# Kernel tuning notes

Hardware: AMD Instinct MI355X
Metric: run time of the kernel (lower is better)

The kernel has to match this reference:

```python
import jax, jax.numpy as jnp
import numpy as np

B = 1024
FEATURE_NUM = 13 + 26 * 4000  # 104013 (13 dense + 26 sparse fields, one-hot dim 4000 each)
FIELD_NUM = 13 + 26           # 39
K = 8


def setup_inputs() -> dict:
    key = jax.random.key(0)
    k1, k2, k3 = jax.random.split(key, 3)
    inputs = jax.random.uniform(k1, (B, FEATURE_NUM), dtype=jnp.float32)
    w0 = jnp.zeros((1,), dtype=jnp.float32)
    w = jax.random.normal(k2, (FEATURE_NUM, 1), dtype=jnp.float32) * 0.05
    v = jax.random.normal(k3, (FEATURE_NUM, FIELD_NUM, K), dtype=jnp.float32) * 0.05
    return {"inputs": inputs, "w0": w0, "w": w, "v": v}


def reference(inputs, w0, w, v):
    # linear part: [B, 1]
    linear_part = w0 + inputs @ w
    # field_f: [B, field_num, K] via tensordot over feature axis
    field_f = jnp.tensordot(inputs, v, axes=1)
    # sum over upper triangle (i<j) of <field_f_i, field_f_j> using the
    # sum-square FM identity: 0.5 * (||sum_i f_i||^2 - sum_i ||f_i||^2)
    s = field_f.sum(axis=1)                       # [B, K]
    inter = 0.5 * (jnp.sum(s * s, axis=-1)
                   - jnp.sum(field_f * field_f, axis=(1, 2)))  # [B]
    return linear_part + inter[:, None]           # [B, 1]
```

## Files before the change

kernel.cpp:

```cpp
#include <hip/hip_runtime.h>
#include <stdint.h>

#define B_SZ 1024
#define F_SZ 104013
#define NFIELD 39
#define N_RAW 312
#define N_PAD 320
#define KB_STEPS 3251
#define PART_ELEMS ((size_t)B_SZ * N_PAD)

using bf16x8 = __attribute__((ext_vector_type(8))) short;
using f32x4  = __attribute__((ext_vector_type(4))) float;

typedef __attribute__((address_space(3))) void* lds_vp;
typedef const __attribute__((address_space(1))) void* glb_cvp;

__device__ __forceinline__ void ld16(const void* g, void* l) {
  __builtin_amdgcn_global_load_lds((glb_cvp)g, (lds_vp)l, 16, 0, 0);
}

__device__ __forceinline__ unsigned int pack_bf16(float a, float b) {
  unsigned int ua = __float_as_uint(a) + 0x8000u;
  unsigned int ub = __float_as_uint(b) + 0x8000u;
  return (ua >> 16) | (ub & 0xffff0000u);
}

__global__ __launch_bounds__(256) void pack_v(const float* __restrict__ v,
                                              const float* __restrict__ w,
                                              uint4* __restrict__ Bp) {
  const int kb = blockIdx.x;
  const int t  = threadIdx.x;
  __shared__ float vs[32][324];

  for (int idx = t; idx < 32 * 78; idx += 256) {
    int r = idx / 78, c4 = (idx % 78) * 4;
    int k = kb * 32 + r;
    float4 val = make_float4(0.f, 0.f, 0.f, 0.f);
    if (k < F_SZ) val = *(const float4*)(v + (size_t)k * N_RAW + c4);
    *(float4*)&vs[r][c4] = val;
  }
  if (t < 32) {
    int k = kb * 32 + t;
    vs[t][312] = (k < F_SZ) ? w[k] : 0.f;
#pragma unroll
    for (int c = 313; c < 320; ++c) vs[t][c] = 0.f;
  }
  __syncthreads();

#pragma unroll
  for (int i = 0; i < 5; ++i) {
    int p  = t + 256 * i;
    int l  = p & 63;
    int kr = (l >> 4) * 8;
    int col = (p >> 6) * 16 + (l & 15);
    uint4 o;
    o.x = pack_bf16(vs[kr + 0][col], vs[kr + 1][col]);
    o.y = pack_bf16(vs[kr + 2][col], vs[kr + 3][col]);
    o.z = pack_bf16(vs[kr + 4][col], vs[kr + 5][col]);
    o.w = pack_bf16(vs[kr + 6][col], vs[kr + 7][col]);
    Bp[(size_t)kb * 1280 + p] = o;
  }
}

#define LDS_BUF 30720
#define B_OFF   10240

__global__ __launch_bounds__(512, 2) void gemm_split(const float* __restrict__ A,
                                                     const uint4* __restrict__ Bp,
                                                     float* __restrict__ part) {
  const int S  = gridDim.x;
  const int s  = blockIdx.x, mt = blockIdx.y;
  const int t  = threadIdx.x;
  const int w  = t >> 6, l = t & 63;
  const int wr = w >> 2, wc = w & 3;
  const int lm = l & 15, lq = l >> 4;
  const int row0 = mt * 128;
  const int kb0 = (int)((long long)KB_STEPS * s / S);
  const int kb1 = (int)((long long)KB_STEPS * (s + 1) / S);

  __shared__ __align__(16) char smem[2][LDS_BUF];

  const int srow = t >> 2, seg = t & 3;
  const float* ag = A + (size_t)(row0 + srow) * F_SZ + seg * 8;
  const int wswz = srow * 80 + ((seg ^ (srow & 3)) << 4);

  auto loadA = [&](int kb, float4& d0, float4& d1) {
    const float* ap = ag + (size_t)kb * 32;
    if (kb != KB_STEPS - 1) {
      d0 = *(const float4*)(ap);
      d1 = *(const float4*)(ap + 4);
    } else {
      const int kbase = kb * 32 + seg * 8;
      float f[8];
#pragma unroll
      for (int e = 0; e < 8; ++e) f[e] = (kbase + e < F_SZ) ? ap[e] : 0.f;
      d0 = make_float4(f[0], f[1], f[2], f[3]);
      d1 = make_float4(f[4], f[5], f[6], f[7]);
    }
  };

  auto writeA = [&](int buf, const float4& d0, const float4& d1) {
    uint4 pk;
    pk.x = pack_bf16(d0.x, d0.y);
    pk.y = pack_bf16(d0.z, d0.w);
    pk.z = pack_bf16(d1.x, d1.y);
    pk.w = pack_bf16(d1.z, d1.w);
    *(uint4*)(smem[buf] + wswz) = pk;
  };

  auto stageB = [&](int kb, int buf) {
    for (int c = w; c < 20; c += 8)
      ld16(Bp + ((size_t)kb * 20 + c) * 64 + l, smem[buf] + B_OFF + c * 1024);
  };

  f32x4 acc[4][5];
#pragma unroll
  for (int i = 0; i < 4; ++i)
#pragma unroll
    for (int n = 0; n < 5; ++n) acc[i][n] = (f32x4)0.f;

  auto compute = [&](int buf) {
    const char* bs = smem[buf];
    bf16x8 af[4];
#pragma unroll
    for (int i = 0; i < 4; ++i)
      af[i] = __builtin_bit_cast(
          bf16x8, *(const uint4*)(bs + (wr * 64 + i * 16 + lm) * 80 +
                                  ((lq ^ (lm & 3)) << 4)));
#pragma unroll
    for (int n = 0; n < 5; ++n) {
      bf16x8 bf = __builtin_bit_cast(
          bf16x8, *(const uint4*)(bs + B_OFF + (wc * 5 + n) * 1024 + l * 16));
#pragma unroll
      for (int i = 0; i < 4; ++i)
        acc[i][n] = __builtin_amdgcn_mfma_f32_16x16x32_bf16(af[i], bf,
                                                            acc[i][n], 0, 0, 0);
    }
  };

  float4 a0, a1, b0, b1;
  loadA(kb0, a0, a1);
  stageB(kb0, 0);
  writeA(0, a0, a1);
  if (kb0 + 1 < kb1) loadA(kb0 + 1, b0, b1);
  __syncthreads();

  int kb = kb0, cur = 0;
  while (true) {
    if (kb + 1 < kb1) {
      stageB(kb + 1, cur ^ 1);
      writeA(cur ^ 1, b0, b1);
      if (kb + 2 < kb1) loadA(kb + 2, a0, a1);
    }
    compute(cur);
    __syncthreads();
    ++kb; cur ^= 1;
    if (kb >= kb1) break;

    if (kb + 1 < kb1) {
      stageB(kb + 1, cur ^ 1);
      writeA(cur ^ 1, a0, a1);
      if (kb + 2 < kb1) loadA(kb + 2, b0, b1);
    }
    compute(cur);
    __syncthreads();
    ++kb; cur ^= 1;
    if (kb >= kb1) break;
  }

  float* outp = part + (size_t)s * PART_ELEMS;
#pragma unroll
  for (int i = 0; i < 4; ++i) {
    int rb = row0 + wr * 64 + i * 16 + lq * 4;
#pragma unroll
    for (int n = 0; n < 5; ++n) {
      int col = (wc * 5 + n) * 16 + lm;
#pragma unroll
      for (int r = 0; r < 4; ++r)
        outp[(size_t)(rb + r) * N_PAD + col] = acc[i][n][r];
    }
  }
}

__global__ __launch_bounds__(320) void finalize(const float* __restrict__ part,
                                                const float* __restrict__ w0,
                                                float* __restrict__ out, int S) {
  const int b = blockIdx.x;
  const int t = threadIdx.x;
  __shared__ float crow[N_PAD];
  __shared__ float red[5];
  __shared__ float skl[8];

  float acc = 0.f;
  const float* p = part + (size_t)b * N_PAD + t;
#pragma unroll 4
  for (int s = 0; s < S; ++s) acc += p[(size_t)s * PART_ELEMS];
  crow[t] = acc;

  float sq = (t < N_RAW) ? acc * acc : 0.f;
#pragma unroll
  for (int off = 32; off; off >>= 1) sq += __shfl_down(sq, off);
  if ((t & 63) == 0) red[t >> 6] = sq;
  __syncthreads();

  if (t < 8) {
    float sk = 0.f;
#pragma unroll
    for (int f = 0; f < NFIELD; ++f) sk += crow[f * 8 + t];
    skl[t] = sk;
  }
  __syncthreads();
  if (t == 0) {
    float sumsq = red[0] + red[1] + red[2] + red[3] + red[4];
    float ss = 0.f;
#pragma unroll
    for (int k = 0; k < 8; ++k) ss += skl[k] * skl[k];
    out[b] = w0[0] + crow[312] + 0.5f * (ss - sumsq);
  }
}

extern "C" void kernel_launch(void* const* d_in, const int* in_sizes, int n_in,
                              void* d_out, int out_size, void* d_ws, size_t ws_size,
                              hipStream_t stream) {
  const float* inputs = (const float*)d_in[0];
  const float* w0 = (const float*)d_in[1];
  const float* w  = (const float*)d_in[2];
  const float* v  = (const float*)d_in[3];
  float* out = (float*)d_out;

  const size_t PART_BYTES   = PART_ELEMS * sizeof(float);
  const size_t PACKED_BYTES = (size_t)KB_STEPS * 20 * 64 * 16;
  int S = 32;
  while (S > 1 && PACKED_BYTES + (size_t)S * PART_BYTES > ws_size) S >>= 1;

  float* part = (float*)d_ws;
  uint4* Bp   = (uint4*)((char*)d_ws + (size_t)S * PART_BYTES);

  pack_v<<<dim3(KB_STEPS), 256, 0, stream>>>(v, w, Bp);
  gemm_split<<<dim3(S, 8), 512, 0, stream>>>(inputs, Bp, part);
  finalize<<<dim3(B_SZ), 320, 0, stream>>>(part, w0, out, S);
}
```

Before: 737.0 us.

## Triple-buffer LDS and deepen prefetch pipeline with explicit vmcnt waits

The GEMM main loop moves from double-buffered LDS with a full __syncthreads to three LDS stages. A is prefetched into registers three k-blocks ahead and B is staged two ahead. Barriers become explicit s_waitcnt vmcnt(N) plus s_barrier, so outstanding global loads can stay in flight across iterations. The packed B layout is padded from 20 to 24 chunks per k-block so each wave issues a fixed three async loads, which adds zero padding and more LDS per block (raising the risk of lower occupancy) and more packed-buffer traffic.

```diff
diff --git a/kernel.cpp b/kernel.cpp
--- a/kernel.cpp
+++ b/kernel.cpp
@@ -7,6 +7,7 @@
 #define N_RAW 312
 #define N_PAD 320
 #define KB_STEPS 3251
+#define BCH 24
 #define PART_ELEMS ((size_t)B_SZ * N_PAD)
 
 using bf16x8 = __attribute__((ext_vector_type(8))) short;
@@ -58,12 +59,20 @@
     o.y = pack_bf16(vs[kr + 2][col], vs[kr + 3][col]);
     o.z = pack_bf16(vs[kr + 4][col], vs[kr + 5][col]);
     o.w = pack_bf16(vs[kr + 6][col], vs[kr + 7][col]);
-    Bp[(size_t)kb * 1280 + p] = o;
-  }
-}
-
-#define LDS_BUF 30720
-#define B_OFF   10240
+    Bp[(size_t)kb * (BCH * 64) + p] = o;
+  }
+  Bp[(size_t)kb * (BCH * 64) + 1280 + t] = make_uint4(0u, 0u, 0u, 0u);
+}
+
+#define LDS_A   10240
+#define LDS_BSZ 24576
+#define LDS_BUF (LDS_A + LDS_BSZ)
+
+#define SYNC(N) do {                                                     \
+    asm volatile("s_waitcnt vmcnt(" #N ") lgkmcnt(0)" ::: "memory");     \
+    __builtin_amdgcn_s_barrier();                                        \
+    __builtin_amdgcn_sched_barrier(0);                                   \
+  } while (0)
 
 __global__ __launch_bounds__(512, 2) void gemm_split(const float* __restrict__ A,
                                                      const uint4* __restrict__ Bp,
@@ -78,7 +87,7 @@
   const int kb0 = (int)((long long)KB_STEPS * s / S);
   const int kb1 = (int)((long long)KB_STEPS * (s + 1) / S);
 
-  __shared__ __align__(16) char smem[2][LDS_BUF];
+  __shared__ __align__(16) char smem[3][LDS_BUF];
 
   const int srow = t >> 2, seg = t & 3;
   const float* ag = A + (size_t)(row0 + srow) * F_SZ + seg * 8;
@@ -109,8 +118,11 @@
   };
 
   auto stageB = [&](int kb, int buf) {
-    for (int c = w; c < 20; c += 8)
-      ld16(Bp + ((size_t)kb * 20 + c) * 64 + l, smem[buf] + B_OFF + c * 1024);
+#pragma unroll
+    for (int j = 0; j < 3; ++j) {
+      int c = w * 3 + j;
+      ld16(Bp + ((size_t)kb * BCH + c) * 64 + l, smem[buf] + LDS_A + c * 1024);
+    }
   };
 
   f32x4 acc[4][5];
@@ -130,7 +142,7 @@
 #pragma unroll
     for (int n = 0; n < 5; ++n) {
       bf16x8 bf = __builtin_bit_cast(
-          bf16x8, *(const uint4*)(bs + B_OFF + (wc * 5 + n) * 1024 + l * 16));
+          bf16x8, *(const uint4*)(bs + LDS_A + (wc * 5 + n) * 1024 + l * 16));
 #pragma unroll
       for (int i = 0; i < 4; ++i)
         acc[i][n] = __builtin_amdgcn_mfma_f32_16x16x32_bf16(af[i], bf,
@@ -138,35 +150,39 @@
     }
   };
 
-  float4 a0, a1, b0, b1;
-  loadA(kb0, a0, a1);
+  float4 s0a, s0b, s1a, s1b, s2a, s2b;
+  loadA(kb0, s0a, s0b);
   stageB(kb0, 0);
-  writeA(0, a0, a1);
-  if (kb0 + 1 < kb1) loadA(kb0 + 1, b0, b1);
-  __syncthreads();
-
-  int kb = kb0, cur = 0;
+  writeA(0, s0a, s0b);
+  loadA(kb0 + 1, s1a, s1b);
+  stageB(kb0 + 1, 1);
+  writeA(1, s1a, s1b);
+  loadA(kb0 + 2, s2a, s2b);
+  loadA(kb0 + 3, s0a, s0b);
+  SYNC(4);
+
+  int kb = kb0;
+#define STEP(BW, SWa, SWb, SLa, SLb, BC) do {                            \
+    if (kb + 2 < kb1) { stageB(kb + 2, BW); writeA(BW, SWa, SWb); }      \
+    if (kb + 4 < kb1) loadA(kb + 4, SLa, SLb);                           \
+    compute(BC);                                                         \
+    int rem = kb1 - kb;                                                  \
+    if (rem > 4) SYNC(7);                                                \
+    else if (rem == 4) SYNC(5);                                          \
+    else if (rem == 3) SYNC(3);                                          \
+    else SYNC(0);                                                        \
+    ++kb;                                                                \
+  } while (0)
+
   while (true) {
-    if (kb + 1 < kb1) {
-      stageB(kb + 1, cur ^ 1);
-      writeA(cur ^ 1, b0, b1);
-      if (kb + 2 < kb1) loadA(kb + 2, a0, a1);
-    }
-    compute(cur);
-    __syncthreads();
-    ++kb; cur ^= 1;
+    STEP(2, s2a, s2b, s1a, s1b, 0);
     if (kb >= kb1) break;
-
-    if (kb + 1 < kb1) {
-      stageB(kb + 1, cur ^ 1);
-      writeA(cur ^ 1, a0, a1);
-      if (kb + 2 < kb1) loadA(kb + 2, b0, b1);
-    }
-    compute(cur);
-    __syncthreads();
-    ++kb; cur ^= 1;
+    STEP(0, s0a, s0b, s2a, s2b, 1);
     if (kb >= kb1) break;
-  }
+    STEP(1, s1a, s1b, s0a, s0b, 2);
+    if (kb >= kb1) break;
+  }
+#undef STEP
 
   float* outp = part + (size_t)s * PART_ELEMS;
 #pragma unroll
@@ -229,7 +245,7 @@
   float* out = (float*)d_out;
 
   const size_t PART_BYTES   = PART_ELEMS * sizeof(float);
-  const size_t PACKED_BYTES = (size_t)KB_STEPS * 20 * 64 * 16;
+  const size_t PACKED_BYTES = (size_t)KB_STEPS * BCH * 64 * 16;
   int S = 32;
   while (S > 1 && PACKED_BYTES + (size_t)S * PART_BYTES > ws_size) S >>= 1;
 
```

Result: slower. 773.5 us (+5.0%).
